# Performance work log

Measured on AMD Instinct MI355X. Metric: run time of the kernel, lower is better.

## Reference

```python
import jax, jax.numpy as jnp
import numpy as np

H = 8   # num_heads
D = 64  # out_features per head

def setup_inputs() -> dict:
    key = jax.random.key(0)
    k1, k2, k3, k4 = jax.random.split(key, 4)
    B, N, F_IN, E = 2, 8192, 512, 65536
    x = jax.random.normal(k1, (B, N, F_IN), dtype=jnp.float32)
    edge_indices = jax.random.randint(k2, (2, E), 0, N)
    W = jax.random.normal(k3, (H * D, F_IN), dtype=jnp.float32) * (1.0 / np.sqrt(F_IN))
    a = jax.random.normal(k4, (2 * D, 1), dtype=jnp.float32) * 0.1
    return {"x": x, "edge_indices": edge_indices, "W": W, "a": a}

def reference(x, edge_indices, W, a):
    # Faithful translation of GraphAttentionLayer.forward (eval mode: dropout = identity).
    B, N, _ = x.shape
    h = (x @ W.T).reshape(B, N, H, D)              # [B,N,H,D]
    src, dst = edge_indices[0], edge_indices[1]
    E = src.shape[0]
    h_src = h[:, src]                               # [B,E,H,D]
    h_dst = h[:, dst]                               # [B,E,H,D]
    # cat([h_src,h_dst]) @ a  ==  h_src @ a[:D] + h_dst @ a[D:]
    a1, a2 = a[:D, 0], a[D:, 0]
    scores = jnp.einsum('behd,d->beh', h_src, a1) + jnp.einsum('behd,d->beh', h_dst, a2)
    scores = jax.nn.leaky_relu(scores, negative_slope=0.2)      # [B,E,H]
    # NOTE: original code softmaxes over the BATCH dim (dim=0) per edge.
    sm = jax.nn.softmax(scores, axis=0)                          # [B,E,H]
    last_edge = jnp.full((N,), -1, dtype=jnp.int32).at[src].max(
        jnp.arange(E, dtype=jnp.int32))                          # [N]
    has_edge = last_edge >= 0
    w = jnp.where(has_edge[None, :, None],
                  sm[:, jnp.clip(last_edge, 0)], 0.0)            # [B,N,H]
    # aggregated[:, s] += w[:, s, :, None] * h_dst[:, e] for each edge e with src[e]==s
    # (weights fully built before aggregation loop) => w[s] * segment_sum(h_dst over src)
    agg_dst = jnp.zeros((B, N, H, D), dtype=h.dtype).at[:, src].add(h_dst)
    aggregated = w[..., None] * agg_dst                          # [B,N,H,D]
    return aggregated.mean(axis=2)                               # [B,N,D]
```

## Files before the change

### kernel.cpp

```cpp
#include <hip/hip_runtime.h>
#include <stdint.h>

#define H_HEADS 8
#define DDIM 64
#define NNODES 8192
#define BB 2
#define FIN 512
#define FOUT 512
#define EDGES 65536
#define CAP 32

typedef unsigned short u16;
typedef unsigned int u32;
typedef __bf16 bf16x8 __attribute__((ext_vector_type(8)));
typedef float f32x4 __attribute__((ext_vector_type(4)));

__device__ __forceinline__ u16 f2bf(float f) {
    u32 u = __float_as_uint(f);
    return (u16)((u + 0x7FFFu + ((u >> 16) & 1u)) >> 16);
}
__device__ __forceinline__ float bf2f(u32 s) {
    return __uint_as_float(s << 16);
}
__device__ __forceinline__ uint4 pack8(float4 a, float4 b) {
    return make_uint4(f2bf(a.x) | ((u32)f2bf(a.y) << 16),
                      f2bf(a.z) | ((u32)f2bf(a.w) << 16),
                      f2bf(b.x) | ((u32)f2bf(b.y) << 16),
                      f2bf(b.z) | ((u32)f2bf(b.w) << 16));
}

#define NEB 64
#define NWB (FOUT * FIN / 8 / 256)
#define NXB (BB * NNODES * FIN / 8 / 256)
__global__ __launch_bounds__(256) void prep_kernel(
    const float* __restrict__ W, const float* __restrict__ X,
    const int* __restrict__ src, const int* __restrict__ dst,
    u16* __restrict__ Wb, u16* __restrict__ Xb,
    int* __restrict__ cursor, int* __restrict__ le_pack,
    int* __restrict__ csr_dst) {
    int blk = blockIdx.x;
    if (blk < NEB) {
        int t = blk * 256 + threadIdx.x;
#pragma unroll
        for (int k = 0; k < 4; k++) {
            int e = t * 4 + k;
            int s = src[e], d = dst[e];
            int slot = atomicAdd(&cursor[s], 1);
            if (slot < CAP) csr_dst[(size_t)s * CAP + slot] = d;
            atomicMax(&le_pack[s], (e << 13) | d);
        }
    } else if (blk < NEB + NWB) {
        int i = (blk - NEB) * 256 + threadIdx.x;
        const float4* p = (const float4*)W;
        float4 v0 = p[(size_t)i * 2], v1 = p[(size_t)i * 2 + 1];
        ((uint4*)Wb)[i] = pack8(v0, v1);
    } else {
        int i = (blk - NEB - NWB) * 256 + threadIdx.x;
        const float4* p = (const float4*)X;
        float4 v0 = p[(size_t)i * 2], v1 = p[(size_t)i * 2 + 1];
        ((uint4*)Xb)[i] = pack8(v0, v1);
    }
}

#define GLDS(g, l)                                                              \
    __builtin_amdgcn_global_load_lds(                                           \
        (const __attribute__((address_space(1))) u32*)(g),                      \
        (__attribute__((address_space(3))) u32*)(l), 16, 0, 0)

__global__ __launch_bounds__(256) void gemm_mfma(const u16* __restrict__ Am,
                                                 const u16* __restrict__ Bm,
                                                 const float* __restrict__ a,
                                                 u16* __restrict__ C,
                                                 float* __restrict__ s1,
                                                 float* __restrict__ s2) {
    __shared__ u16 As[3][128 * 32];
    __shared__ u16 Bs[3][128 * 32];
    int tid = threadIdx.x;
    int gb = blockIdx.x;
    int m_idx = (gb & 7) | ((gb >> 5) << 3);
    int n_idx = (gb >> 3) & 3;
    int m0 = m_idx * 128, n0 = n_idx * 128;
    int lane = tid & 63, wv = tid >> 6;
    int wr = (wv >> 1) * 64, wc = (wv & 1) * 64;
    int l15 = lane & 15, quad = lane >> 4;
    f32x4 acc[4][4] = {};

    int srow = tid >> 2;
    int scol = (tid & 3) * 8;
    const u16* Ag = Am + (size_t)(m0 + srow) * FIN + scol;
    const u16* Bg = Bm + (size_t)(n0 + srow) * FIN + scol;

#define STAGE(c, kk)                                                            \
    do {                                                                        \
        u16* Al_ = As[c] + tid * 8;                                             \
        u16* Bl_ = Bs[c] + tid * 8;                                             \
        GLDS(Ag + (kk), Al_);                                                   \
        GLDS(Ag + (kk) + (size_t)64 * FIN, Al_ + 64 * 32);                      \
        GLDS(Bg + (kk), Bl_);                                                   \
        GLDS(Bg + (kk) + (size_t)64 * FIN, Bl_ + 64 * 32);                      \
    } while (0)

#define COMPUTE(c)                                                              \
    do {                                                                        \
        bf16x8 af[4], bfr[4];                                                   \
        _Pragma("unroll") for (int i = 0; i < 4; i++) af[i] =                   \
            *(const bf16x8*)(As[c] + (wr + i * 16 + l15) * 32 + quad * 8);      \
        _Pragma("unroll") for (int j = 0; j < 4; j++) bfr[j] =                  \
            *(const bf16x8*)(Bs[c] + (wc + j * 16 + l15) * 32 + quad * 8);      \
        _Pragma("unroll") for (int i = 0; i < 4; i++)                           \
            _Pragma("unroll") for (int j = 0; j < 4; j++) acc[i][j] =           \
                __builtin_amdgcn_mfma_f32_16x16x32_bf16(af[i], bfr[j],          \
                                                        acc[i][j], 0, 0, 0);    \
    } while (0)

    STAGE(0, 0);
    STAGE(1, 32);
    int c0 = 0, c2 = 2;
#pragma unroll 1
    for (int t = 0; t < 14; ++t) {
        asm volatile("s_waitcnt vmcnt(4)" ::: "memory");
        __builtin_amdgcn_s_barrier();
        __builtin_amdgcn_sched_barrier(0);
        STAGE(c2, (t + 2) * 32);
        COMPUTE(c0);
        c0 = (c0 == 2) ? 0 : c0 + 1;
        c2 = (c2 == 2) ? 0 : c2 + 1;
    }
    asm volatile("s_waitcnt vmcnt(4)" ::: "memory");
    __builtin_amdgcn_s_barrier();
    __builtin_amdgcn_sched_barrier(0);
    COMPUTE(2);
    asm volatile("s_waitcnt vmcnt(0)" ::: "memory");
    __builtin_amdgcn_s_barrier();
    __builtin_amdgcn_sched_barrier(0);
    COMPUTE(0);

#pragma unroll
    for (int i = 0; i < 4; i++) {
        int row_base = m0 + wr + i * 16 + quad * 4;
#pragma unroll
        for (int j = 0; j < 4; j++) {
            int col = n0 + wc + j * 16 + l15;
#pragma unroll
            for (int r = 0; r < 4; r++)
                C[(size_t)(row_base + r) * FOUT + col] = f2bf(acc[i][j][r]);
        }
    }

    float a1v[4], a2v[4];
#pragma unroll
    for (int j = 0; j < 4; j++) {
        a1v[j] = a[j * 16 + l15];
        a2v[j] = a[DDIM + j * 16 + l15];
    }
    int head = n_idx * 2 + (wv & 1);
#pragma unroll
    for (int i = 0; i < 4; i++) {
#pragma unroll
        for (int r = 0; r < 4; r++) {
            float p1 = 0.f, p2 = 0.f;
#pragma unroll
            for (int j = 0; j < 4; j++) {
                p1 += a1v[j] * acc[i][j][r];
                p2 += a2v[j] * acc[i][j][r];
            }
#pragma unroll
            for (int m = 1; m <= 8; m <<= 1) {
                p1 += __shfl_xor(p1, m);
                p2 += __shfl_xor(p2, m);
            }
            if (l15 == 0) {
                int row = m0 + wr + i * 16 + quad * 4 + r;
                s1[row * H_HEADS + head] = p1;
                s2[row * H_HEADS + head] = p2;
            }
        }
    }
}

__device__ __forceinline__ void acc8(float* acc, uint4 v) {
    acc[0] += bf2f(v.x & 0xffffu);
    acc[1] += bf2f(v.x >> 16);
    acc[2] += bf2f(v.y & 0xffffu);
    acc[3] += bf2f(v.y >> 16);
    acc[4] += bf2f(v.z & 0xffffu);
    acc[5] += bf2f(v.z >> 16);
    acc[6] += bf2f(v.w & 0xffffu);
    acc[7] += bf2f(v.w >> 16);
}

__global__ __launch_bounds__(256) void aggregate(const u16* __restrict__ h,
                                                 const float* __restrict__ s1,
                                                 const float* __restrict__ s2,
                                                 const int* __restrict__ cursor,
                                                 const int* __restrict__ le_pack,
                                                 const int* __restrict__ csr_dst,
                                                 float* __restrict__ out, int N) {
    int n = blockIdx.x * 2 + (threadIdx.x >> 7);
    int b = (threadIdx.x >> 6) & 1;
    int lane = threadIdx.x & 63;
    int head = lane >> 3;

    int deg = cursor[n];
    deg = deg < CAP ? deg : CAP;
    int pk = le_pack[n];

    const int* cp = csr_dst + (size_t)n * CAP;
    int myidx = (lane < CAP) ? cp[lane] : 0;

    float wgt = 0.f;
    if (deg > 0) {
        int dl = pk & 8191;
        float sc0 = s1[(0 * N + n) * H_HEADS + head] +
                    s2[((size_t)0 * N + dl) * H_HEADS + head];
        float sc1 = s1[((size_t)1 * N + n) * H_HEADS + head] +
                    s2[((size_t)1 * N + dl) * H_HEADS + head];
        sc0 = sc0 >= 0.f ? sc0 : 0.2f * sc0;
        sc1 = sc1 >= 0.f ? sc1 : 0.2f * sc1;
        float m = fmaxf(sc0, sc1);
        float e0 = __expf(sc0 - m), e1 = __expf(sc1 - m);
        wgt = (b == 0 ? e0 : e1) / (e0 + e1);
    }

    float acc[8] = {};
    const u16* hb = h + (size_t)b * N * FOUT + lane * 8;
    int degm = deg & ~3;
    for (int j0 = 0; j0 < degm; j0 += 4) {
        int d0 = __shfl(myidx, j0);
        int d1 = __shfl(myidx, j0 + 1);
        int d2 = __shfl(myidx, j0 + 2);
        int d3 = __shfl(myidx, j0 + 3);
        uint4 v0 = *(const uint4*)(hb + (size_t)d0 * FOUT);
        uint4 v1 = *(const uint4*)(hb + (size_t)d1 * FOUT);
        uint4 v2 = *(const uint4*)(hb + (size_t)d2 * FOUT);
        uint4 v3 = *(const uint4*)(hb + (size_t)d3 * FOUT);
        acc8(acc, v0);
        acc8(acc, v1);
        acc8(acc, v2);
        acc8(acc, v3);
    }
    for (int j = degm; j < deg; j++) {
        int dn = __shfl(myidx, j);
        uint4 v = *(const uint4*)(hb + (size_t)dn * FOUT);
        acc8(acc, v);
    }

    float val[8];
#pragma unroll
    for (int k = 0; k < 8; k++) val[k] = acc[k] * wgt;
#pragma unroll
    for (int m = 8; m <= 32; m <<= 1)
#pragma unroll
        for (int k = 0; k < 8; k++) val[k] += __shfl_xor(val[k], m);
    if (lane < 8) {
        float* op = out + ((size_t)b * N + n) * DDIM + lane * 8;
        const float inv = 1.0f / H_HEADS;
        *(float4*)op = make_float4(val[0] * inv, val[1] * inv, val[2] * inv,
                                   val[3] * inv);
        *(float4*)(op + 4) = make_float4(val[4] * inv, val[5] * inv,
                                         val[6] * inv, val[7] * inv);
    }
}

extern "C" void kernel_launch(void* const* d_in, const int* in_sizes, int n_in,
                              void* d_out, int out_size, void* d_ws,
                              size_t ws_size, hipStream_t stream) {
    const float* x = (const float*)d_in[0];
    const int* edges = (const int*)d_in[1];
    const float* W = (const float*)d_in[2];
    const float* a = (const float*)d_in[3];
    float* out = (float*)d_out;

    const int* src = edges;
    const int* dst = edges + EDGES;

    char* p = (char*)d_ws;
    auto carve = [&](size_t bytes) {
        char* r = p;
        p += (bytes + 255) & ~(size_t)255;
        return r;
    };
    u16* Wb = (u16*)carve((size_t)FOUT * FIN * 2);
    u16* Xb = (u16*)carve((size_t)BB * NNODES * FIN * 2);
    u16* h = (u16*)carve((size_t)BB * NNODES * FOUT * 2);
    float* s1 = (float*)carve((size_t)BB * NNODES * H_HEADS * 4);
    float* s2 = (float*)carve((size_t)BB * NNODES * H_HEADS * 4);
    int* cursor = (int*)carve(NNODES * 4);
    int* le_pack = (int*)carve(NNODES * 4);
    int* csr_dst = (int*)carve((size_t)NNODES * CAP * 4);

    const int M = BB * NNODES;

    hipMemsetAsync(cursor, 0, 2 * NNODES * 4, stream);
    prep_kernel<<<NEB + NWB + NXB, 256, 0, stream>>>(W, x, src, dst, Wb, Xb,
                                                     cursor, le_pack, csr_dst);
    gemm_mfma<<<(M / 128) * (FOUT / 128), 256, 0, stream>>>(Xb, Wb, a, h, s1,
                                                            s2);
    aggregate<<<NNODES / 2, 256, 0, stream>>>(h, s1, s2, cursor, le_pack,
                                              csr_dst, out, NNODES);
}
```

Baseline: 125.6 us.

## Fuse X fp32-to-bf16 conversion into GEMM with swizzled fp32 LDS staging

The separate prep pass that converted X to bf16 is removed. The GEMM now streams fp32 X tiles straight into LDS with an XOR swizzle and converts them to bf16 just before the MFMA. This avoids writing and re-reading a 16 MB bf16 copy of X, at the cost of twice the LDS footprint for A, more global-to-LDS load instructions per stage, and conversion ALU work in the inner loop. The aggregate gather loop is also restructured into a single predicated 4-way unrolled loop with no scalar tail.

```diff
diff --git a/kernel.cpp b/kernel.cpp
--- a/kernel.cpp
+++ b/kernel.cpp
@@ -31,11 +31,9 @@
 
 #define NEB 64
 #define NWB (FOUT * FIN / 8 / 256)
-#define NXB (BB * NNODES * FIN / 8 / 256)
 __global__ __launch_bounds__(256) void prep_kernel(
-    const float* __restrict__ W, const float* __restrict__ X,
-    const int* __restrict__ src, const int* __restrict__ dst,
-    u16* __restrict__ Wb, u16* __restrict__ Xb,
+    const float* __restrict__ W, const int* __restrict__ src,
+    const int* __restrict__ dst, u16* __restrict__ Wb,
     int* __restrict__ cursor, int* __restrict__ le_pack,
     int* __restrict__ csr_dst) {
     int blk = blockIdx.x;
@@ -49,16 +47,11 @@
             if (slot < CAP) csr_dst[(size_t)s * CAP + slot] = d;
             atomicMax(&le_pack[s], (e << 13) | d);
         }
-    } else if (blk < NEB + NWB) {
+    } else {
         int i = (blk - NEB) * 256 + threadIdx.x;
         const float4* p = (const float4*)W;
         float4 v0 = p[(size_t)i * 2], v1 = p[(size_t)i * 2 + 1];
         ((uint4*)Wb)[i] = pack8(v0, v1);
-    } else {
-        int i = (blk - NEB - NWB) * 256 + threadIdx.x;
-        const float4* p = (const float4*)X;
-        float4 v0 = p[(size_t)i * 2], v1 = p[(size_t)i * 2 + 1];
-        ((uint4*)Xb)[i] = pack8(v0, v1);
     }
 }
 
@@ -67,14 +60,14 @@
         (const __attribute__((address_space(1))) u32*)(g),                      \
         (__attribute__((address_space(3))) u32*)(l), 16, 0, 0)
 
-__global__ __launch_bounds__(256) void gemm_mfma(const u16* __restrict__ Am,
+__global__ __launch_bounds__(256) void gemm_mfma(const float* __restrict__ X,
                                                  const u16* __restrict__ Bm,
                                                  const float* __restrict__ a,
                                                  u16* __restrict__ C,
                                                  float* __restrict__ s1,
                                                  float* __restrict__ s2) {
-    __shared__ u16 As[3][128 * 32];
-    __shared__ u16 Bs[3][128 * 32];
+    __shared__ __align__(16) float AsF[3][128 * 32];
+    __shared__ __align__(16) u16 Bs[3][128 * 32];
     int tid = threadIdx.x;
     int gb = blockIdx.x;
     int m_idx = (gb & 7) | ((gb >> 5) << 3);
@@ -85,17 +78,22 @@
     int l15 = lane & 15, quad = lane >> 4;
     f32x4 acc[4][4] = {};
 
-    int srow = tid >> 2;
-    int scol = (tid & 3) * 8;
-    const u16* Ag = Am + (size_t)(m0 + srow) * FIN + scol;
-    const u16* Bg = Bm + (size_t)(n0 + srow) * FIN + scol;
+    int srA = tid >> 3;
+    int scA = ((tid & 7) ^ (srA & 7)) * 4;
+    const float* AgSw = X + (size_t)(m0 + srA) * FIN + scA;
+
+    int srB = tid >> 2;
+    int scB = (tid & 3) * 8;
+    const u16* Bg = Bm + (size_t)(n0 + srB) * FIN + scB;
 
 #define STAGE(c, kk)                                                            \
     do {                                                                        \
-        u16* Al_ = As[c] + tid * 8;                                             \
+        float* Al_ = AsF[c] + tid * 4;                                          \
         u16* Bl_ = Bs[c] + tid * 8;                                             \
-        GLDS(Ag + (kk), Al_);                                                   \
-        GLDS(Ag + (kk) + (size_t)64 * FIN, Al_ + 64 * 32);                      \
+        GLDS(AgSw + (kk), Al_);                                                 \
+        GLDS(AgSw + (kk) + (size_t)32 * FIN, Al_ + 32 * 32);                    \
+        GLDS(AgSw + (kk) + (size_t)64 * FIN, Al_ + 64 * 32);                    \
+        GLDS(AgSw + (kk) + (size_t)96 * FIN, Al_ + 96 * 32);                    \
         GLDS(Bg + (kk), Bl_);                                                   \
         GLDS(Bg + (kk) + (size_t)64 * FIN, Bl_ + 64 * 32);                      \
     } while (0)
@@ -103,8 +101,19 @@
 #define COMPUTE(c)                                                              \
     do {                                                                        \
         bf16x8 af[4], bfr[4];                                                   \
-        _Pragma("unroll") for (int i = 0; i < 4; i++) af[i] =                   \
-            *(const bf16x8*)(As[c] + (wr + i * 16 + l15) * 32 + quad * 8);      \
+        _Pragma("unroll") for (int i = 0; i < 4; i++) {                         \
+            int r_ = wr + i * 16 + l15;                                         \
+            const float* bp_ = AsF[c] + r_ * 32;                                \
+            int sx_ = r_ & 7;                                                   \
+            f32x4 v0_ = *(const f32x4*)(bp_ + (((quad * 2 + 0) ^ sx_) << 2));   \
+            f32x4 v1_ = *(const f32x4*)(bp_ + (((quad * 2 + 1) ^ sx_) << 2));   \
+            bf16x8 t_;                                                          \
+            t_[0] = (__bf16)v0_[0]; t_[1] = (__bf16)v0_[1];                     \
+            t_[2] = (__bf16)v0_[2]; t_[3] = (__bf16)v0_[3];                     \
+            t_[4] = (__bf16)v1_[0]; t_[5] = (__bf16)v1_[1];                     \
+            t_[6] = (__bf16)v1_[2]; t_[7] = (__bf16)v1_[3];                     \
+            af[i] = t_;                                                         \
+        }                                                                       \
         _Pragma("unroll") for (int j = 0; j < 4; j++) bfr[j] =                  \
             *(const bf16x8*)(Bs[c] + (wc + j * 16 + l15) * 32 + quad * 8);      \
         _Pragma("unroll") for (int i = 0; i < 4; i++)                           \
@@ -118,7 +127,7 @@
     int c0 = 0, c2 = 2;
 #pragma unroll 1
     for (int t = 0; t < 14; ++t) {
-        asm volatile("s_waitcnt vmcnt(4)" ::: "memory");
+        asm volatile("s_waitcnt vmcnt(6)" ::: "memory");
         __builtin_amdgcn_s_barrier();
         __builtin_amdgcn_sched_barrier(0);
         STAGE(c2, (t + 2) * 32);
@@ -126,7 +135,7 @@
         c0 = (c0 == 2) ? 0 : c0 + 1;
         c2 = (c2 == 2) ? 0 : c2 + 1;
     }
-    asm volatile("s_waitcnt vmcnt(4)" ::: "memory");
+    asm volatile("s_waitcnt vmcnt(6)" ::: "memory");
     __builtin_amdgcn_s_barrier();
     __builtin_amdgcn_sched_barrier(0);
     COMPUTE(2);
@@ -176,17 +185,6 @@
             }
         }
     }
-}
-
-__device__ __forceinline__ void acc8(float* acc, uint4 v) {
-    acc[0] += bf2f(v.x & 0xffffu);
-    acc[1] += bf2f(v.x >> 16);
-    acc[2] += bf2f(v.y & 0xffffu);
-    acc[3] += bf2f(v.y >> 16);
-    acc[4] += bf2f(v.z & 0xffffu);
-    acc[5] += bf2f(v.z >> 16);
-    acc[6] += bf2f(v.w & 0xffffu);
-    acc[7] += bf2f(v.w >> 16);
 }
 
 __global__ __launch_bounds__(256) void aggregate(const u16* __restrict__ h,
@@ -224,25 +222,22 @@
 
     float acc[8] = {};
     const u16* hb = h + (size_t)b * N * FOUT + lane * 8;
-    int degm = deg & ~3;
-    for (int j0 = 0; j0 < degm; j0 += 4) {
-        int d0 = __shfl(myidx, j0);
-        int d1 = __shfl(myidx, j0 + 1);
-        int d2 = __shfl(myidx, j0 + 2);
-        int d3 = __shfl(myidx, j0 + 3);
-        uint4 v0 = *(const uint4*)(hb + (size_t)d0 * FOUT);
-        uint4 v1 = *(const uint4*)(hb + (size_t)d1 * FOUT);
-        uint4 v2 = *(const uint4*)(hb + (size_t)d2 * FOUT);
-        uint4 v3 = *(const uint4*)(hb + (size_t)d3 * FOUT);
-        acc8(acc, v0);
-        acc8(acc, v1);
-        acc8(acc, v2);
-        acc8(acc, v3);
-    }
-    for (int j = degm; j < deg; j++) {
-        int dn = __shfl(myidx, j);
-        uint4 v = *(const uint4*)(hb + (size_t)dn * FOUT);
-        acc8(acc, v);
+    for (int j0 = 0; j0 < deg; j0 += 4) {
+#pragma unroll
+        for (int k = 0; k < 4; k++) {
+            int j = j0 + k;
+            float f = (j < deg) ? 1.0f : 0.0f;
+            int dn = (j < deg) ? __shfl(myidx, j) : 0;
+            uint4 v = *(const uint4*)(hb + (size_t)dn * FOUT);
+            acc[0] = fmaf(f, bf2f(v.x & 0xffffu), acc[0]);
+            acc[1] = fmaf(f, bf2f(v.x >> 16), acc[1]);
+            acc[2] = fmaf(f, bf2f(v.y & 0xffffu), acc[2]);
+            acc[3] = fmaf(f, bf2f(v.y >> 16), acc[3]);
+            acc[4] = fmaf(f, bf2f(v.z & 0xffffu), acc[4]);
+            acc[5] = fmaf(f, bf2f(v.z >> 16), acc[5]);
+            acc[6] = fmaf(f, bf2f(v.w & 0xffffu), acc[6]);
+            acc[7] = fmaf(f, bf2f(v.w >> 16), acc[7]);
+        }
     }
 
     float val[8];
@@ -281,7 +276,6 @@
         return r;
     };
     u16* Wb = (u16*)carve((size_t)FOUT * FIN * 2);
-    u16* Xb = (u16*)carve((size_t)BB * NNODES * FIN * 2);
     u16* h = (u16*)carve((size_t)BB * NNODES * FOUT * 2);
     float* s1 = (float*)carve((size_t)BB * NNODES * H_HEADS * 4);
     float* s2 = (float*)carve((size_t)BB * NNODES * H_HEADS * 4);
@@ -292,9 +286,9 @@
     const int M = BB * NNODES;
 
     hipMemsetAsync(cursor, 0, 2 * NNODES * 4, stream);
-    prep_kernel<<<NEB + NWB + NXB, 256, 0, stream>>>(W, x, src, dst, Wb, Xb,
-                                                     cursor, le_pack, csr_dst);
-    gemm_mfma<<<(M / 128) * (FOUT / 128), 256, 0, stream>>>(Xb, Wb, a, h, s1,
+    prep_kernel<<<NEB + NWB, 256, 0, stream>>>(W, src, dst, Wb, cursor,
+                                               le_pack, csr_dst);
+    gemm_mfma<<<(M / 128) * (FOUT / 128), 256, 0, stream>>>(x, Wb, a, h, s1,
                                                             s2);
     aggregate<<<NNODES / 2, 256, 0, stream>>>(h, s1, s2, cursor, le_pack,
                                               csr_dst, out, NNODES);
```

Result: no change. 127.3 us (+1.3%).
